# Kernel optimization log

Measured on AMD Instinct MI355X. Metric: run time of the kernel, lower is better.

Reference implementation:

```python
import jax, jax.numpy as jnp
import numpy as np

B, H, W, C = 8, 64, 64, 64
C8 = C // 8

def setup_inputs() -> dict:
    key = jax.random.key(0)
    ks = jax.random.split(key, 5)
    x = jax.random.normal(ks[0], (B, H, W, C), dtype=jnp.float32)
    # 1x1 conv kernels (fan-in scaled) + biases
    wq = jax.random.normal(ks[1], (C, C8), dtype=jnp.float32) / np.sqrt(C)
    wk = jax.random.normal(ks[2], (C, C8), dtype=jnp.float32) / np.sqrt(C)
    wv = jax.random.normal(ks[3], (C, C), dtype=jnp.float32) / np.sqrt(C)
    bq = jnp.zeros((C8,), dtype=jnp.float32)
    bk = jnp.zeros((C8,), dtype=jnp.float32)
    bv = jnp.zeros((C,), dtype=jnp.float32)
    gamma = jax.random.normal(ks[4], (), dtype=jnp.float32)
    return {"x": x, "wq": wq, "bq": bq, "wk": wk, "bk": bk,
            "wv": wv, "bv": bv, "gamma": gamma}

def reference(x, wq, bq, wk, bk, wv, bv, gamma):
    b, h, w, c = x.shape
    n = h * w
    # 1x1 convs == per-pixel linear projections
    q = (jnp.einsum('bhwc,cd->bhwd', x, wq) + bq).reshape(b, n, -1)  # [B,N,C/8]
    k = (jnp.einsum('bhwc,cd->bhwd', x, wk) + bk).reshape(b, n, -1)  # [B,N,C/8]
    v = (jnp.einsum('bhwc,cd->bhwd', x, wv) + bv).reshape(b, n, -1)  # [B,N,C]
    # Unscaled attention: softmax over keys (last axis), no 1/sqrt(d)
    attn = jax.nn.softmax(jnp.einsum('bnd,bmd->bnm', q, k), axis=-1)  # [B,N,N]
    out = jnp.einsum('bnm,bmc->bnc', attn, v).reshape(b, h, w, c)
    return out * gamma + x
```

## Files before the change

### kernel.cpp

```cpp
#include <hip/hip_runtime.h>
#include <hip/hip_bf16.h>


#define BB 8
#define NN 4096
#define CC 64
#define PSTRIDE 72
#define LOG2E 1.44269504088896f

typedef _Float16 f16;
typedef _Float16 half8 __attribute__((ext_vector_type(8)));
typedef _Float16 half4 __attribute__((ext_vector_type(4)));
typedef __fp16 fp16x2 __attribute__((ext_vector_type(2)));
typedef float floatx4 __attribute__((ext_vector_type(4)));

static __device__ inline half4 pack4(float a, float b, float c, float d) {
    fp16x2 lo = __builtin_amdgcn_cvt_pkrtz(a, b);
    fp16x2 hi = __builtin_amdgcn_cvt_pkrtz(c, d);
    unsigned int lou = __builtin_bit_cast(unsigned int, lo);
    unsigned int hiu = __builtin_bit_cast(unsigned int, hi);
    unsigned long long packed = (unsigned long long)lou | ((unsigned long long)hiu << 32);
    return __builtin_bit_cast(half4, packed);
}


__global__ __launch_bounds__(256) void proj_all_kernel(
    const float* __restrict__ x,
    const float* __restrict__ wq, const float* __restrict__ bq,
    const float* __restrict__ wk, const float* __restrict__ bk,
    const float* __restrict__ wv, const float* __restrict__ bv,
    f16* __restrict__ Qh, f16* __restrict__ Kf, f16* __restrict__ Vf,
    float* __restrict__ qn2, float* __restrict__ kn2)
{
    __shared__ alignas(16) f16 Ws[80][PSTRIDE];
    __shared__ float Bs[80];
    __shared__ alignas(16) f16 Vs[64][68];
    __shared__ alignas(16) f16 Ks[64][12];
    const int tid = threadIdx.x;

    for (int i = tid; i < 4096; i += 256) {
        int cin = i >> 6, cout = i & 63;
        Ws[cout][cin] = (f16)wv[i];
    }
    for (int i = tid; i < 512; i += 256) {
        int cin = i >> 3, c = i & 7;
        Ws[64 + c][cin] = (f16)(wq[i] * LOG2E);
        Ws[72 + c][cin] = (f16)wk[i];
    }
    if (tid < 80)
        Bs[tid] = (tid < 64) ? bv[tid]
                : (tid < 72 ? bq[tid - 64] * LOG2E : bk[tid - 72]);
    __syncthreads();

    const int wave = tid >> 6, lane = tid & 63;
    const int quad = lane >> 4, n16 = lane & 15;
    const long pb = (long)blockIdx.x * 64;
    const long p0 = pb + wave * 16;
    const int  b   = (int)(pb >> 12);
    const int  nnb = (int)(pb & 4095);

    half8 ax[2];
#pragma unroll
    for (int kh = 0; kh < 2; ++kh) {
        const float* xp = x + (p0 + n16) * 64 + kh * 32 + quad * 8;
        float4 x1 = *(const float4*)xp;
        float4 x2 = *(const float4*)(xp + 4);
        ax[kh][0] = (f16)x1.x; ax[kh][1] = (f16)x1.y;
        ax[kh][2] = (f16)x1.z; ax[kh][3] = (f16)x1.w;
        ax[kh][4] = (f16)x2.x; ax[kh][5] = (f16)x2.y;
        ax[kh][6] = (f16)x2.z; ax[kh][7] = (f16)x2.w;
    }

#pragma unroll
    for (int ct = 0; ct < 5; ++ct) {
        const int cout = (ct < 4) ? ct * 16 + n16 : 64 + n16;
        const float bias = Bs[cout];
        half8 b0 = *(const half8*)(&Ws[cout][quad * 8]);
        half8 b1 = *(const half8*)(&Ws[cout][32 + quad * 8]);
        floatx4 acc = {bias, bias, bias, bias};
        acc = __builtin_amdgcn_mfma_f32_16x16x32_f16(ax[0], b0, acc, 0, 0, 0);
        acc = __builtin_amdgcn_mfma_f32_16x16x32_f16(ax[1], b1, acc, 0, 0, 0);
        if (ct < 4) {
#pragma unroll
            for (int r = 0; r < 4; ++r)
                Vs[wave * 16 + quad * 4 + r][ct * 16 + n16] = (f16)acc[r];
        } else {
            float n2[4];
#pragma unroll
            for (int r = 0; r < 4; ++r) n2[r] = acc[r] * acc[r];
#pragma unroll
            for (int d = 1; d < 8; d <<= 1)
#pragma unroll
                for (int r = 0; r < 4; ++r) n2[r] += __shfl_xor(n2[r], d, 64);
            if (n16 == 0) {
#pragma unroll
                for (int r = 0; r < 4; ++r) qn2[p0 + quad * 4 + r] = n2[r];
            } else if (n16 == 8) {
#pragma unroll
                for (int r = 0; r < 4; ++r) kn2[p0 + quad * 4 + r] = n2[r];
            }
            if (n16 < 8) {
                f16* dst = Qh + (p0 + quad * 4) * 8 + n16;
#pragma unroll
                for (int r = 0; r < 4; ++r) dst[r * 8] = (f16)acc[r];
            } else {
#pragma unroll
                for (int r = 0; r < 4; ++r)
                    Ks[wave * 16 + quad * 4 + r][n16 - 8] = (f16)acc[r];
            }
        }
    }
    __syncthreads();

#pragma unroll
    for (int u = 0; u < 2; ++u) {
        const int tt = wave * 2 + u;
        const int kb = tt >> 2, ct = tt & 3;
        half8 v;
#pragma unroll
        for (int j = 0; j < 8; ++j)
            v[j] = Vs[kb * 32 + quad * 8 + j][ct * 16 + n16];
        const size_t kbg = (size_t)b * 128 + (nnb >> 5) + kb;
        *(half8*)(Vf + (kbg * 4 + ct) * 512 + lane * 8) = v;
    }
    if (wave < 2) {
        half8 kp;
#pragma unroll
        for (int e = 0; e < 2; ++e) {
            const int t = wave * 2 + e;
#pragma unroll
            for (int j = 0; j < 4; ++j) {
                f16 v = (f16)0.f;
                if (quad < 2) v = Ks[t * 16 + n16][quad * 4 + j];
                else if (quad == 2 && j == 0) v = (f16)1.f;
                kp[e * 4 + j] = v;
            }
        }
        const size_t kpg = (size_t)b * 128 + (nnb >> 5) + wave;
        *(half8*)(Kf + kpg * 512 + lane * 8) = kp;
    }
}

__global__ __launch_bounds__(256) void knorm_max_kernel(
    const float* __restrict__ kn2, float* __restrict__ Mk2)
{
    __shared__ float red[4];
    const int b = blockIdx.x, tid = threadIdx.x;
    float mx = 0.f;
    for (int i = tid; i < NN; i += 256) mx = fmaxf(mx, kn2[(size_t)b * NN + i]);
#pragma unroll
    for (int d = 1; d < 64; d <<= 1) mx = fmaxf(mx, __shfl_xor(mx, d, 64));
    if ((tid & 63) == 0) red[tid >> 6] = mx;
    __syncthreads();
    if (tid == 0) Mk2[b] = fmaxf(fmaxf(red[0], red[1]), fmaxf(red[2], red[3]));
}

__global__ __launch_bounds__(256, 3) void attn_kernel(
    const f16* __restrict__ Qh, const f16* __restrict__ Kf,
    const f16* __restrict__ Vf,
    const float* __restrict__ qn2, const float* __restrict__ Mk2,
    const float* __restrict__ x, const float* __restrict__ gptr,
    float* __restrict__ out)
{
    __shared__ alignas(16) char smem[24576];
    f16*   Pbuf = (f16*)smem;
    float* Obuf = (float*)smem;
    __shared__ float Ls[4][2][16];

    const int tid  = threadIdx.x;
    const int wave = tid >> 6, lane = tid & 63;
    const int quad = lane >> 4, n16 = lane & 15;
    const int ks = wave;

    const int b  = blockIdx.x & 7;
    const int qt = blockIdx.x >> 3;
    const size_t bN = (size_t)b * NN;

    const float mk2 = Mk2[b];

    half4 bq4[2];
#pragma unroll
    for (int qt2 = 0; qt2 < 2; ++qt2) {
        const int q = qt * 32 + qt2 * 16 + n16;
        const float mf = __builtin_sqrtf(qn2[bN + q] * mk2) - 12.0f;
        half4 v = {0, 0, 0, 0};
        if (quad < 2)
            v = *(const half4*)(Qh + (bN + q) * 8 + quad * 4);
        else if (quad == 2)
            v[0] = (f16)(-mf);
        bq4[qt2] = v;
    }

    floatx4 oacc[2][4];
#pragma unroll
    for (int qt2 = 0; qt2 < 2; ++qt2)
#pragma unroll
        for (int ct = 0; ct < 4; ++ct) oacc[qt2][ct] = (floatx4){0.f, 0.f, 0.f, 0.f};
    float l_loc[2] = {0.f, 0.f};

    const f16* kfb = Kf + ((size_t)b * 128 + ks * 32) * 512;
    const f16* vfb = Vf + ((size_t)b * 128 + ks * 32) * 2048;
    const floatx4 zero4 = {0.f, 0.f, 0.f, 0.f};
    f16* Pw0 = Pbuf + (wave * 2 + 0) * 16 * PSTRIDE;
    f16* Pw1 = Pbuf + (wave * 2 + 1) * 16 * PSTRIDE;

    for (int it = 0; it < 16; ++it) {
        half8 kk0 = *(const half8*)(kfb + (size_t)(it * 2 + 0) * 512 + lane * 8);
        half8 kk1 = *(const half8*)(kfb + (size_t)(it * 2 + 1) * 512 + lane * 8);
        half8 av0[4], av1[4];
#pragma unroll
        for (int ct = 0; ct < 4; ++ct)
            av0[ct] = *(const half8*)(vfb + ((size_t)(it * 2) * 4 + ct) * 512 + lane * 8);
#pragma unroll
        for (int ct = 0; ct < 4; ++ct)
            av1[ct] = *(const half8*)(vfb + ((size_t)(it * 2 + 1) * 4 + ct) * 512 + lane * 8);

        half4 ak[4];
        ak[0] = __builtin_shufflevector(kk0, kk0, 0, 1, 2, 3);
        ak[1] = __builtin_shufflevector(kk0, kk0, 4, 5, 6, 7);
        ak[2] = __builtin_shufflevector(kk1, kk1, 0, 1, 2, 3);
        ak[3] = __builtin_shufflevector(kk1, kk1, 4, 5, 6, 7);

        floatx4 sf[4];
#pragma unroll
        for (int t = 0; t < 4; ++t)
            sf[t] = __builtin_amdgcn_mfma_f32_16x16x16f16(ak[t], bq4[0], zero4, 0, 0, 0);

#pragma unroll
        for (int qt2 = 0; qt2 < 2; ++qt2) {
            if (qt2 == 1) {
#pragma unroll
                for (int t = 0; t < 4; ++t)
                    sf[t] = __builtin_amdgcn_mfma_f32_16x16x16f16(ak[t], bq4[1], zero4, 0, 0, 0);
            }
            float rst[4];
#pragma unroll
            for (int t = 0; t < 4; ++t) {
                float pv0 = __builtin_exp2f(sf[t][0]);
                float pv1 = __builtin_exp2f(sf[t][1]);
                float pv2 = __builtin_exp2f(sf[t][2]);
                float pv3 = __builtin_exp2f(sf[t][3]);
                sf[t][0] = pv0; sf[t][1] = pv1; sf[t][2] = pv2; sf[t][3] = pv3;
                rst[t] = (pv0 + pv1) + (pv2 + pv3);
            }
            l_loc[qt2] += (rst[0] + rst[1]) + (rst[2] + rst[3]);
            f16* Pw = qt2 ? Pw1 : Pw0;
#pragma unroll
            for (int t = 0; t < 4; ++t) {
                half4 pk = pack4(sf[t][0], sf[t][1], sf[t][2], sf[t][3]);
                *(half4*)(Pw + n16 * PSTRIDE + t * 16 + quad * 4) = pk;
            }
        }
        __asm__ volatile("s_waitcnt lgkmcnt(0)" ::: "memory");

#pragma unroll
        for (int qt2 = 0; qt2 < 2; ++qt2) {
            f16* Pw = qt2 ? Pw1 : Pw0;
            half8 bp0 = *(const half8*)(Pw + n16 * PSTRIDE + quad * 8);
            half8 bp1 = *(const half8*)(Pw + n16 * PSTRIDE + 32 + quad * 8);
#pragma unroll
            for (int ct = 0; ct < 4; ++ct)
                oacc[qt2][ct] = __builtin_amdgcn_mfma_f32_16x16x32_f16(av0[ct], bp0, oacc[qt2][ct], 0, 0, 0);
#pragma unroll
            for (int ct = 0; ct < 4; ++ct)
                oacc[qt2][ct] = __builtin_amdgcn_mfma_f32_16x16x32_f16(av1[ct], bp1, oacc[qt2][ct], 0, 0, 0);
        }
    }

    float l_run[2];
#pragma unroll
    for (int qt2 = 0; qt2 < 2; ++qt2) {
        float l = l_loc[qt2];
        l += __shfl_xor(l, 16, 64);
        l += __shfl_xor(l, 32, 64);
        l_run[qt2] = l;
    }

    __syncthreads();
    if (ks > 0) {
#pragma unroll
        for (int qt2 = 0; qt2 < 2; ++qt2) {
            if (quad == 0) Ls[ks][qt2][n16] = l_run[qt2];
            float* ob = Obuf + (((ks - 1) * 2 + qt2) * 64 + lane) * 16;
#pragma unroll
            for (int ct = 0; ct < 4; ++ct)
                *(floatx4*)(ob + ct * 4) = oacc[qt2][ct];
        }
    }
    __syncthreads();
    if (ks == 0) {
        const float g = gptr[0];
#pragma unroll
        for (int qt2 = 0; qt2 < 2; ++qt2) {
            float l = l_run[qt2];
            float o[16];
#pragma unroll
            for (int ct = 0; ct < 4; ++ct)
#pragma unroll
                for (int r = 0; r < 4; ++r) o[ct * 4 + r] = oacc[qt2][ct][r];
#pragma unroll
            for (int p = 1; p < 4; ++p) {
                l += Ls[p][qt2][n16];
                const float* ob = Obuf + (((p - 1) * 2 + qt2) * 64 + lane) * 16;
#pragma unroll
                for (int i = 0; i < 16; ++i) o[i] += ob[i];
            }
            const float scale = g / l;
            const int q = qt * 32 + qt2 * 16 + n16;
#pragma unroll
            for (int ct = 0; ct < 4; ++ct) {
                const size_t idx = (bN + q) * CC + ct * 16 + quad * 4;
                float4 xr = *(const float4*)(x + idx);
                float4 res;
                res.x = o[ct * 4 + 0] * scale + xr.x;
                res.y = o[ct * 4 + 1] * scale + xr.y;
                res.z = o[ct * 4 + 2] * scale + xr.z;
                res.w = o[ct * 4 + 3] * scale + xr.w;
                *(float4*)(out + idx) = res;
            }
        }
    }
}

extern "C" void kernel_launch(void* const* d_in, const int* in_sizes, int n_in,
                              void* d_out, int out_size, void* d_ws, size_t ws_size,
                              hipStream_t stream) {
    const float* x     = (const float*)d_in[0];
    const float* wq    = (const float*)d_in[1];
    const float* bq    = (const float*)d_in[2];
    const float* wk    = (const float*)d_in[3];
    const float* bk    = (const float*)d_in[4];
    const float* wv    = (const float*)d_in[5];
    const float* bv    = (const float*)d_in[6];
    const float* gamma = (const float*)d_in[7];
    float* out = (float*)d_out;

    f16* Qh = (f16*)d_ws;
    f16* Kf = Qh + (size_t)BB * NN * 8;
    f16* Vf = Kf + (size_t)BB * 128 * 512;
    float* qn2 = (float*)(Vf + (size_t)BB * 128 * 4 * 512);
    float* kn2 = qn2 + (size_t)BB * NN;
    float* Mk2 = kn2 + (size_t)BB * NN;

    proj_all_kernel<<<512, 256, 0, stream>>>(x, wq, bq, wk, bk, wv, bv,
                                             Qh, Kf, Vf, qn2, kn2);
    knorm_max_kernel<<<BB, 256, 0, stream>>>(kn2, Mk2);
    attn_kernel<<<BB * 128, 256, 0, stream>>>(Qh, Kf, Vf, qn2, Mk2, x, gamma, out);
}
```

Baseline: 129.7 us.

## Feed softmax probabilities directly from registers into PV MFMA, dropping LDS round-trip

The V fragment layout written by the projection kernel is reordered so that the C-layout output of the QK^T MFMA can be used directly as the B operand of 16x16x16 MFMAs for P·V. This removes the per-iteration LDS write/read of P and the lgkmcnt wait. The attention block is narrowed to 16 queries (grid doubled, occupancy hint raised to 4), which halves register use per block but means K/V fragments are reloaded by twice as many blocks. PV now uses 16 smaller MFMAs per iteration instead of 8 larger ones.

```diff
diff --git a/kernel.cpp b/kernel.cpp
--- a/kernel.cpp
+++ b/kernel.cpp
@@ -115,13 +115,15 @@
 #pragma unroll
     for (int u = 0; u < 2; ++u) {
         const int tt = wave * 2 + u;
-        const int kb = tt >> 2, ct = tt & 3;
+        const int p  = tt >> 2, ct = tt & 3;
         half8 v;
 #pragma unroll
-        for (int j = 0; j < 8; ++j)
-            v[j] = Vs[kb * 32 + quad * 8 + j][ct * 16 + n16];
-        const size_t kbg = (size_t)b * 128 + (nnb >> 5) + kb;
-        *(half8*)(Vf + (kbg * 4 + ct) * 512 + lane * 8) = v;
+        for (int e = 0; e < 2; ++e)
+#pragma unroll
+            for (int j = 0; j < 4; ++j)
+                v[e * 4 + j] = Vs[p * 32 + e * 16 + quad * 4 + j][ct * 16 + n16];
+        const size_t pg = (size_t)b * 128 + (nnb >> 5) + p;
+        *(half8*)(Vf + (pg * 4 + ct) * 512 + lane * 8) = v;
     }
     if (wave < 2) {
         half8 kp;
@@ -155,17 +157,15 @@
     if (tid == 0) Mk2[b] = fmaxf(fmaxf(red[0], red[1]), fmaxf(red[2], red[3]));
 }
 
-__global__ __launch_bounds__(256, 3) void attn_kernel(
+__global__ __launch_bounds__(256, 4) void attn_kernel(
     const f16* __restrict__ Qh, const f16* __restrict__ Kf,
     const f16* __restrict__ Vf,
     const float* __restrict__ qn2, const float* __restrict__ Mk2,
     const float* __restrict__ x, const float* __restrict__ gptr,
     float* __restrict__ out)
 {
-    __shared__ alignas(16) char smem[24576];
-    f16*   Pbuf = (f16*)smem;
-    float* Obuf = (float*)smem;
-    __shared__ float Ls[4][2][16];
+    __shared__ alignas(16) float Obuf[3][64][16];
+    __shared__ float Ls[4][16];
 
     const int tid  = threadIdx.x;
     const int wave = tid >> 6, lane = tid & 63;
@@ -174,46 +174,34 @@
 
     const int b  = blockIdx.x & 7;
     const int qt = blockIdx.x >> 3;
+    const int q  = qt * 16 + n16;
     const size_t bN = (size_t)b * NN;
 
-    const float mk2 = Mk2[b];
-
-    half4 bq4[2];
-#pragma unroll
-    for (int qt2 = 0; qt2 < 2; ++qt2) {
-        const int q = qt * 32 + qt2 * 16 + n16;
-        const float mf = __builtin_sqrtf(qn2[bN + q] * mk2) - 12.0f;
-        half4 v = {0, 0, 0, 0};
-        if (quad < 2)
-            v = *(const half4*)(Qh + (bN + q) * 8 + quad * 4);
-        else if (quad == 2)
-            v[0] = (f16)(-mf);
-        bq4[qt2] = v;
-    }
-
-    floatx4 oacc[2][4];
-#pragma unroll
-    for (int qt2 = 0; qt2 < 2; ++qt2)
-#pragma unroll
-        for (int ct = 0; ct < 4; ++ct) oacc[qt2][ct] = (floatx4){0.f, 0.f, 0.f, 0.f};
-    float l_loc[2] = {0.f, 0.f};
+    const float mf = __builtin_sqrtf(qn2[bN + q] * Mk2[b]) - 12.0f;
+    half4 bq4 = {0, 0, 0, 0};
+    if (quad < 2)
+        bq4 = *(const half4*)(Qh + (bN + q) * 8 + quad * 4);
+    else if (quad == 2)
+        bq4[0] = (f16)(-mf);
+
+    floatx4 oacc[4];
+#pragma unroll
+    for (int ct = 0; ct < 4; ++ct) oacc[ct] = (floatx4){0.f, 0.f, 0.f, 0.f};
+    float l_loc = 0.f;
 
     const f16* kfb = Kf + ((size_t)b * 128 + ks * 32) * 512;
     const f16* vfb = Vf + ((size_t)b * 128 + ks * 32) * 2048;
     const floatx4 zero4 = {0.f, 0.f, 0.f, 0.f};
-    f16* Pw0 = Pbuf + (wave * 2 + 0) * 16 * PSTRIDE;
-    f16* Pw1 = Pbuf + (wave * 2 + 1) * 16 * PSTRIDE;
 
     for (int it = 0; it < 16; ++it) {
         half8 kk0 = *(const half8*)(kfb + (size_t)(it * 2 + 0) * 512 + lane * 8);
         half8 kk1 = *(const half8*)(kfb + (size_t)(it * 2 + 1) * 512 + lane * 8);
-        half8 av0[4], av1[4];
-#pragma unroll
-        for (int ct = 0; ct < 4; ++ct)
-            av0[ct] = *(const half8*)(vfb + ((size_t)(it * 2) * 4 + ct) * 512 + lane * 8);
-#pragma unroll
-        for (int ct = 0; ct < 4; ++ct)
-            av1[ct] = *(const half8*)(vfb + ((size_t)(it * 2 + 1) * 4 + ct) * 512 + lane * 8);
+        half8 av[2][4];
+#pragma unroll
+        for (int qp = 0; qp < 2; ++qp)
+#pragma unroll
+            for (int ct = 0; ct < 4; ++ct)
+                av[qp][ct] = *(const half8*)(vfb + ((size_t)(it * 2 + qp) * 4 + ct) * 512 + lane * 8);
 
         half4 ak[4];
         ak[0] = __builtin_shufflevector(kk0, kk0, 0, 1, 2, 3);
@@ -224,100 +212,72 @@
         floatx4 sf[4];
 #pragma unroll
         for (int t = 0; t < 4; ++t)
-            sf[t] = __builtin_amdgcn_mfma_f32_16x16x16f16(ak[t], bq4[0], zero4, 0, 0, 0);
-
-#pragma unroll
-        for (int qt2 = 0; qt2 < 2; ++qt2) {
-            if (qt2 == 1) {
-#pragma unroll
-                for (int t = 0; t < 4; ++t)
-                    sf[t] = __builtin_amdgcn_mfma_f32_16x16x16f16(ak[t], bq4[1], zero4, 0, 0, 0);
+            sf[t] = __builtin_amdgcn_mfma_f32_16x16x16f16(ak[t], bq4, zero4, 0, 0, 0);
+
+        float rst[4];
+        half4 pk[4];
+#pragma unroll
+        for (int t = 0; t < 4; ++t) {
+            float pv0 = __builtin_exp2f(sf[t][0]);
+            float pv1 = __builtin_exp2f(sf[t][1]);
+            float pv2 = __builtin_exp2f(sf[t][2]);
+            float pv3 = __builtin_exp2f(sf[t][3]);
+            rst[t] = (pv0 + pv1) + (pv2 + pv3);
+            pk[t] = pack4(pv0, pv1, pv2, pv3);
+        }
+        l_loc += (rst[0] + rst[1]) + (rst[2] + rst[3]);
+
+#pragma unroll
+        for (int t = 0; t < 4; ++t) {
+            const int qp = t >> 1;
+#pragma unroll
+            for (int ct = 0; ct < 4; ++ct) {
+                half4 va = (t & 1)
+                    ? __builtin_shufflevector(av[qp][ct], av[qp][ct], 4, 5, 6, 7)
+                    : __builtin_shufflevector(av[qp][ct], av[qp][ct], 0, 1, 2, 3);
+                oacc[ct] = __builtin_amdgcn_mfma_f32_16x16x16f16(va, pk[t], oacc[ct], 0, 0, 0);
             }
-            float rst[4];
-#pragma unroll
-            for (int t = 0; t < 4; ++t) {
-                float pv0 = __builtin_exp2f(sf[t][0]);
-                float pv1 = __builtin_exp2f(sf[t][1]);
-                float pv2 = __builtin_exp2f(sf[t][2]);
-                float pv3 = __builtin_exp2f(sf[t][3]);
-                sf[t][0] = pv0; sf[t][1] = pv1; sf[t][2] = pv2; sf[t][3] = pv3;
-                rst[t] = (pv0 + pv1) + (pv2 + pv3);
-            }
-            l_loc[qt2] += (rst[0] + rst[1]) + (rst[2] + rst[3]);
-            f16* Pw = qt2 ? Pw1 : Pw0;
-#pragma unroll
-            for (int t = 0; t < 4; ++t) {
-                half4 pk = pack4(sf[t][0], sf[t][1], sf[t][2], sf[t][3]);
-                *(half4*)(Pw + n16 * PSTRIDE + t * 16 + quad * 4) = pk;
-            }
-        }
-        __asm__ volatile("s_waitcnt lgkmcnt(0)" ::: "memory");
-
-#pragma unroll
-        for (int qt2 = 0; qt2 < 2; ++qt2) {
-            f16* Pw = qt2 ? Pw1 : Pw0;
-            half8 bp0 = *(const half8*)(Pw + n16 * PSTRIDE + quad * 8);
-            half8 bp1 = *(const half8*)(Pw + n16 * PSTRIDE + 32 + quad * 8);
-#pragma unroll
-            for (int ct = 0; ct < 4; ++ct)
-                oacc[qt2][ct] = __builtin_amdgcn_mfma_f32_16x16x32_f16(av0[ct], bp0, oacc[qt2][ct], 0, 0, 0);
-#pragma unroll
-            for (int ct = 0; ct < 4; ++ct)
-                oacc[qt2][ct] = __builtin_amdgcn_mfma_f32_16x16x32_f16(av1[ct], bp1, oacc[qt2][ct], 0, 0, 0);
-        }
-    }
-
-    float l_run[2];
-#pragma unroll
-    for (int qt2 = 0; qt2 < 2; ++qt2) {
-        float l = l_loc[qt2];
-        l += __shfl_xor(l, 16, 64);
-        l += __shfl_xor(l, 32, 64);
-        l_run[qt2] = l;
-    }
+        }
+    }
+
+    float l_run = l_loc;
+    l_run += __shfl_xor(l_run, 16, 64);
+    l_run += __shfl_xor(l_run, 32, 64);
 
     __syncthreads();
     if (ks > 0) {
-#pragma unroll
-        for (int qt2 = 0; qt2 < 2; ++qt2) {
-            if (quad == 0) Ls[ks][qt2][n16] = l_run[qt2];
-            float* ob = Obuf + (((ks - 1) * 2 + qt2) * 64 + lane) * 16;
-#pragma unroll
-            for (int ct = 0; ct < 4; ++ct)
-                *(floatx4*)(ob + ct * 4) = oacc[qt2][ct];
-        }
+        if (quad == 0) Ls[ks][n16] = l_run;
+        float* ob = &Obuf[ks - 1][lane][0];
+#pragma unroll
+        for (int ct = 0; ct < 4; ++ct)
+            *(floatx4*)(ob + ct * 4) = oacc[ct];
     }
     __syncthreads();
     if (ks == 0) {
-        const float g = gptr[0];
-#pragma unroll
-        for (int qt2 = 0; qt2 < 2; ++qt2) {
-            float l = l_run[qt2];
-            float o[16];
-#pragma unroll
-            for (int ct = 0; ct < 4; ++ct)
-#pragma unroll
-                for (int r = 0; r < 4; ++r) o[ct * 4 + r] = oacc[qt2][ct][r];
-#pragma unroll
-            for (int p = 1; p < 4; ++p) {
-                l += Ls[p][qt2][n16];
-                const float* ob = Obuf + (((p - 1) * 2 + qt2) * 64 + lane) * 16;
-#pragma unroll
-                for (int i = 0; i < 16; ++i) o[i] += ob[i];
-            }
-            const float scale = g / l;
-            const int q = qt * 32 + qt2 * 16 + n16;
-#pragma unroll
-            for (int ct = 0; ct < 4; ++ct) {
-                const size_t idx = (bN + q) * CC + ct * 16 + quad * 4;
-                float4 xr = *(const float4*)(x + idx);
-                float4 res;
-                res.x = o[ct * 4 + 0] * scale + xr.x;
-                res.y = o[ct * 4 + 1] * scale + xr.y;
-                res.z = o[ct * 4 + 2] * scale + xr.z;
-                res.w = o[ct * 4 + 3] * scale + xr.w;
-                *(float4*)(out + idx) = res;
-            }
+        float l = l_run;
+        float o[16];
+#pragma unroll
+        for (int ct = 0; ct < 4; ++ct)
+#pragma unroll
+            for (int r = 0; r < 4; ++r) o[ct * 4 + r] = oacc[ct][r];
+#pragma unroll
+        for (int p = 1; p < 4; ++p) {
+            l += Ls[p][n16];
+            const float* ob = &Obuf[p - 1][lane][0];
+#pragma unroll
+            for (int i = 0; i < 16; ++i) o[i] += ob[i];
+        }
+        const float scale = gptr[0] / l;
+#pragma unroll
+        for (int ct = 0; ct < 4; ++ct) {
+            const size_t idx = (bN + q) * CC + ct * 16 + quad * 4;
+            float4 xr = *(const float4*)(x + idx);
+            float4 res;
+            res.x = o[ct * 4 + 0] * scale + xr.x;
+            res.y = o[ct * 4 + 1] * scale + xr.y;
+            res.z = o[ct * 4 + 2] * scale + xr.z;
+            res.w = o[ct * 4 + 3] * scale + xr.w;
+            *(float4*)(out + idx) = res;
         }
     }
 }
@@ -345,5 +305,5 @@
     proj_all_kernel<<<512, 256, 0, stream>>>(x, wq, bq, wk, bk, wv, bv,
                                              Qh, Kf, Vf, qn2, kn2);
     knorm_max_kernel<<<BB, 256, 0, stream>>>(kn2, Mk2);
-    attn_kernel<<<BB * 128, 256, 0, stream>>>(Qh, Kf, Vf, qn2, Mk2, x, gamma, out);
-}
+    attn_kernel<<<BB * 256, 256, 0, stream>>>(Qh, Kf, Vf, qn2, Mk2, x, gamma, out);
+}
```

Measured after the change: 135.2 us. +4.2%, slower.

## Feed softmax probabilities to PV MFMA directly from registers, dropping LDS round-trip

Applied to the files above, without the earlier changes.

The QK^T MFMA output layout is reused directly as the B operand of 16x16x16 PV MFMAs, so P no longer goes through an LDS write, wait and read-back each iteration. The V fragment layout written by the projection kernel is permuted to match this register layout. This removes LDS traffic and the lgkmcnt stall from the inner loop. In exchange it issues twice as many smaller MFMAs (16x16x16 instead of 16x16x32), which may lower MFMA throughput.

```diff
diff --git a/kernel.cpp b/kernel.cpp
--- a/kernel.cpp
+++ b/kernel.cpp
@@ -115,13 +115,15 @@
 #pragma unroll
     for (int u = 0; u < 2; ++u) {
         const int tt = wave * 2 + u;
-        const int kb = tt >> 2, ct = tt & 3;
+        const int p  = tt >> 2, ct = tt & 3;
         half8 v;
 #pragma unroll
-        for (int j = 0; j < 8; ++j)
-            v[j] = Vs[kb * 32 + quad * 8 + j][ct * 16 + n16];
-        const size_t kbg = (size_t)b * 128 + (nnb >> 5) + kb;
-        *(half8*)(Vf + (kbg * 4 + ct) * 512 + lane * 8) = v;
+        for (int e = 0; e < 2; ++e)
+#pragma unroll
+            for (int j = 0; j < 4; ++j)
+                v[e * 4 + j] = Vs[p * 32 + e * 16 + quad * 4 + j][ct * 16 + n16];
+        const size_t pg = (size_t)b * 128 + (nnb >> 5) + p;
+        *(half8*)(Vf + (pg * 4 + ct) * 512 + lane * 8) = v;
     }
     if (wave < 2) {
         half8 kp;
@@ -162,9 +164,7 @@
     const float* __restrict__ x, const float* __restrict__ gptr,
     float* __restrict__ out)
 {
-    __shared__ alignas(16) char smem[24576];
-    f16*   Pbuf = (f16*)smem;
-    float* Obuf = (float*)smem;
+    __shared__ alignas(16) float Obuf[3][2][64][16];
     __shared__ float Ls[4][2][16];
 
     const int tid  = threadIdx.x;
@@ -201,19 +201,16 @@
     const f16* kfb = Kf + ((size_t)b * 128 + ks * 32) * 512;
     const f16* vfb = Vf + ((size_t)b * 128 + ks * 32) * 2048;
     const floatx4 zero4 = {0.f, 0.f, 0.f, 0.f};
-    f16* Pw0 = Pbuf + (wave * 2 + 0) * 16 * PSTRIDE;
-    f16* Pw1 = Pbuf + (wave * 2 + 1) * 16 * PSTRIDE;
 
     for (int it = 0; it < 16; ++it) {
         half8 kk0 = *(const half8*)(kfb + (size_t)(it * 2 + 0) * 512 + lane * 8);
         half8 kk1 = *(const half8*)(kfb + (size_t)(it * 2 + 1) * 512 + lane * 8);
-        half8 av0[4], av1[4];
-#pragma unroll
-        for (int ct = 0; ct < 4; ++ct)
-            av0[ct] = *(const half8*)(vfb + ((size_t)(it * 2) * 4 + ct) * 512 + lane * 8);
-#pragma unroll
-        for (int ct = 0; ct < 4; ++ct)
-            av1[ct] = *(const half8*)(vfb + ((size_t)(it * 2 + 1) * 4 + ct) * 512 + lane * 8);
+        half8 av[2][4];
+#pragma unroll
+        for (int qp = 0; qp < 2; ++qp)
+#pragma unroll
+            for (int ct = 0; ct < 4; ++ct)
+                av[qp][ct] = *(const half8*)(vfb + ((size_t)(it * 2 + qp) * 4 + ct) * 512 + lane * 8);
 
         half4 ak[4];
         ak[0] = __builtin_shufflevector(kk0, kk0, 0, 1, 2, 3);
@@ -221,49 +218,37 @@
         ak[2] = __builtin_shufflevector(kk1, kk1, 0, 1, 2, 3);
         ak[3] = __builtin_shufflevector(kk1, kk1, 4, 5, 6, 7);
 
-        floatx4 sf[4];
-#pragma unroll
-        for (int t = 0; t < 4; ++t)
-            sf[t] = __builtin_amdgcn_mfma_f32_16x16x16f16(ak[t], bq4[0], zero4, 0, 0, 0);
-
 #pragma unroll
         for (int qt2 = 0; qt2 < 2; ++qt2) {
-            if (qt2 == 1) {
-#pragma unroll
-                for (int t = 0; t < 4; ++t)
-                    sf[t] = __builtin_amdgcn_mfma_f32_16x16x16f16(ak[t], bq4[1], zero4, 0, 0, 0);
-            }
+            floatx4 sf[4];
+#pragma unroll
+            for (int t = 0; t < 4; ++t)
+                sf[t] = __builtin_amdgcn_mfma_f32_16x16x16f16(ak[t], bq4[qt2], zero4, 0, 0, 0);
+
             float rst[4];
+            half4 pk[4];
 #pragma unroll
             for (int t = 0; t < 4; ++t) {
                 float pv0 = __builtin_exp2f(sf[t][0]);
                 float pv1 = __builtin_exp2f(sf[t][1]);
                 float pv2 = __builtin_exp2f(sf[t][2]);
                 float pv3 = __builtin_exp2f(sf[t][3]);
-                sf[t][0] = pv0; sf[t][1] = pv1; sf[t][2] = pv2; sf[t][3] = pv3;
                 rst[t] = (pv0 + pv1) + (pv2 + pv3);
+                pk[t] = pack4(pv0, pv1, pv2, pv3);
             }
             l_loc[qt2] += (rst[0] + rst[1]) + (rst[2] + rst[3]);
-            f16* Pw = qt2 ? Pw1 : Pw0;
+
 #pragma unroll
             for (int t = 0; t < 4; ++t) {
-                half4 pk = pack4(sf[t][0], sf[t][1], sf[t][2], sf[t][3]);
-                *(half4*)(Pw + n16 * PSTRIDE + t * 16 + quad * 4) = pk;
-            }
-        }
-        __asm__ volatile("s_waitcnt lgkmcnt(0)" ::: "memory");
-
-#pragma unroll
-        for (int qt2 = 0; qt2 < 2; ++qt2) {
-            f16* Pw = qt2 ? Pw1 : Pw0;
-            half8 bp0 = *(const half8*)(Pw + n16 * PSTRIDE + quad * 8);
-            half8 bp1 = *(const half8*)(Pw + n16 * PSTRIDE + 32 + quad * 8);
-#pragma unroll
-            for (int ct = 0; ct < 4; ++ct)
-                oacc[qt2][ct] = __builtin_amdgcn_mfma_f32_16x16x32_f16(av0[ct], bp0, oacc[qt2][ct], 0, 0, 0);
-#pragma unroll
-            for (int ct = 0; ct < 4; ++ct)
-                oacc[qt2][ct] = __builtin_amdgcn_mfma_f32_16x16x32_f16(av1[ct], bp1, oacc[qt2][ct], 0, 0, 0);
+                const int qp = t >> 1;
+#pragma unroll
+                for (int ct = 0; ct < 4; ++ct) {
+                    half4 va = (t & 1)
+                        ? __builtin_shufflevector(av[qp][ct], av[qp][ct], 4, 5, 6, 7)
+                        : __builtin_shufflevector(av[qp][ct], av[qp][ct], 0, 1, 2, 3);
+                    oacc[qt2][ct] = __builtin_amdgcn_mfma_f32_16x16x16f16(va, pk[t], oacc[qt2][ct], 0, 0, 0);
+                }
+            }
         }
     }
 
@@ -281,7 +266,7 @@
 #pragma unroll
         for (int qt2 = 0; qt2 < 2; ++qt2) {
             if (quad == 0) Ls[ks][qt2][n16] = l_run[qt2];
-            float* ob = Obuf + (((ks - 1) * 2 + qt2) * 64 + lane) * 16;
+            float* ob = &Obuf[ks - 1][qt2][lane][0];
 #pragma unroll
             for (int ct = 0; ct < 4; ++ct)
                 *(floatx4*)(ob + ct * 4) = oacc[qt2][ct];
@@ -301,7 +286,7 @@
 #pragma unroll
             for (int p = 1; p < 4; ++p) {
                 l += Ls[p][qt2][n16];
-                const float* ob = Obuf + (((p - 1) * 2 + qt2) * 64 + lane) * 16;
+                const float* ob = &Obuf[p - 1][qt2][lane][0];
 #pragma unroll
                 for (int i = 0; i < 16; ++i) o[i] += ob[i];
             }
```

After: 137.0 us. 5.6% more time.
